# Performance work log

Measured on AMD Instinct MI355X. Metric: run time of the kernel, lower is better.

## Reference

```python
import jax, jax.numpy as jnp
import numpy as np

N_NODES = 100000
N_EDGES = 1600000
DIM = 128
N_SEEDS = 15000


def _gcn_stack(edges, x, Ws):
    """Multi-layer GCN with sym-normalized edge-list aggregation, residual, ReLU.
    edges: [2, E] int; x: [N, d] float; Ws: list of [d, d] weights."""
    n = x.shape[0]
    loop = jnp.arange(n, dtype=edges.dtype)
    src = jnp.concatenate([edges[0], loop])  # add self-loops
    dst = jnp.concatenate([edges[1], loop])
    deg = jax.ops.segment_sum(jnp.ones(src.shape, x.dtype), dst, num_segments=n)
    dinv = jax.lax.rsqrt(deg)  # deg >= 1 thanks to self-loops
    norm = dinv[src] * dinv[dst]  # [E+N]
    for W in Ws:
        h = x @ W                                   # [N, d] dense transform
        msg = norm[:, None] * h[src]                # gather + scale, [E+N, d]
        agg = jax.ops.segment_sum(msg, dst, num_segments=n)  # scatter-add
        x = jax.nn.relu(agg + h)                    # residual + activation
    return x


def setup_inputs() -> dict:
    key = jax.random.key(0)
    ks = jax.random.split(key, 8)
    scale = 1.0 / np.sqrt(DIM)
    return {
        "sr_ent_seeds": jax.random.randint(ks[0], (N_SEEDS,), 0, N_NODES),
        "tg_ent_seeds": jax.random.randint(ks[1], (N_SEEDS,), 0, N_NODES),
        "edges_sr": jax.random.randint(ks[2], (2, N_EDGES), 0, N_NODES),
        "edges_tg": jax.random.randint(ks[3], (2, N_EDGES), 0, N_NODES),
        "embedding_sr": jax.random.normal(ks[4], (N_NODES, DIM), jnp.float32),
        "embedding_tg": jax.random.normal(ks[5], (N_NODES, DIM), jnp.float32),
        "W0": jax.random.normal(ks[6], (DIM, DIM), jnp.float32) * scale,
        "W1": jax.random.normal(ks[7], (DIM, DIM), jnp.float32) * scale,
    }


def reference(sr_ent_seeds, tg_ent_seeds, edges_sr, edges_tg,
              embedding_sr, embedding_tg, W0, W1):
    Ws = [W0, W1]
    sr_ent_hid = _gcn_stack(edges_sr, embedding_sr, Ws)
    tg_ent_hid = _gcn_stack(edges_tg, embedding_tg, Ws)
    sr_seed_hid = sr_ent_hid[sr_ent_seeds]
    tg_seed_hid = tg_ent_hid[tg_ent_seeds]
    return (sr_seed_hid, tg_seed_hid, sr_ent_hid, tg_ent_hid)
```

## Files before the change

kernel.cpp:

```cpp
#include <hip/hip_runtime.h>

#define NN 100000
#define NE 1600000
#define NT (2 * NN)
#define ET (2 * NE)
#define DIM 128
#define NS 15000
#define SB2 ((NT + 255) / 256)
#define PAD 136
#define NRANGE 8
#define RSZ (NT / NRANGE)
#define CH 32
#define CI4 (ET / 4 / CH)
#define NE4 (NE / 4)

typedef __attribute__((ext_vector_type(8))) short frag_ab;
typedef __attribute__((ext_vector_type(4))) float frag_cd;
typedef __attribute__((ext_vector_type(4))) int i4;

__device__ __forceinline__ unsigned short f2bf(float f) {
    unsigned int u = __float_as_uint(f);
    u += 0x7fff + ((u >> 16) & 1);
    return (unsigned short)(u >> 16);
}
__device__ __forceinline__ float bflo(unsigned int u) { return __uint_as_float(u << 16); }
__device__ __forceinline__ float bfhi(unsigned int u) { return __uint_as_float(u & 0xffff0000u); }

__global__ __launch_bounds__(1024) void hist_k(const int* __restrict__ e_sr,
                                               const int* __restrict__ e_tg,
                                               int* __restrict__ P) {
    __shared__ int lc[RSZ];
    const int r = blockIdx.x & (NRANGE - 1);
    const int c = blockIdx.x >> 3;
    const int lo = r * RSZ;
    for (int i = threadIdx.x; i < RSZ; i += 1024) lc[i] = 0;
    __syncthreads();
    const int base = c * CI4;
    for (int v = threadIdx.x; v < CI4; v += 1024) {
        i4 d4;
        if (c < 16) {
            d4 = *((const i4*)e_sr + NE4 + base + v);
        } else {
            d4 = *((const i4*)e_tg + base + v);
            d4 += NN;
        }
#pragma unroll
        for (int j = 0; j < 4; ++j) {
            const int t = d4[j] - lo;
            if ((unsigned)t < RSZ) atomicAdd(&lc[t], 1);
        }
    }
    __syncthreads();
    for (int i = threadIdx.x; i < RSZ; i += 1024) P[c * NT + lo + i] = lc[i];
}

__global__ __launch_bounds__(256) void reduceA_k(const int* __restrict__ P,
                                                 int* __restrict__ cnt,
                                                 float* __restrict__ dinv,
                                                 int* __restrict__ bsum) {
    __shared__ int sh[256];
    const int t = threadIdx.x;
    const int i = blockIdx.x * 256 + t;
    int s = 0;
    if (i < NT) {
#pragma unroll
        for (int c = 0; c < CH; ++c) s += P[c * NT + i];
        cnt[i] = s;
        dinv[i] = rsqrtf((float)(s + 1));
    }
    sh[t] = s;
    __syncthreads();
    for (int off = 128; off > 0; off >>= 1) {
        if (t < off) sh[t] += sh[t + off];
        __syncthreads();
    }
    if (t == 0) bsum[blockIdx.x] = sh[0];
}

__global__ __launch_bounds__(1024) void scanB_k(int* bsum, int* row_ptr) {
    __shared__ int s[1024];
    const int t = threadIdx.x;
    const int v = (t < SB2) ? bsum[t] : 0;
    s[t] = v;
    __syncthreads();
    for (int off = 1; off < 1024; off <<= 1) {
        int add = (t >= off) ? s[t - off] : 0;
        __syncthreads();
        s[t] += add;
        __syncthreads();
    }
    if (t < SB2) bsum[t] = s[t] - v;
    if (t == SB2 - 1) row_ptr[NT] = s[t];
}

__global__ __launch_bounds__(256) void scanCbase_k(const int* __restrict__ cnt,
                                                   const int* __restrict__ bsum,
                                                   int* __restrict__ row_ptr,
                                                   int* __restrict__ P) {
    __shared__ int s[256];
    const int t = threadIdx.x;
    const int i = blockIdx.x * 256 + t;
    const int v = (i < NT) ? cnt[i] : 0;
    s[t] = v;
    __syncthreads();
    for (int off = 1; off < 256; off <<= 1) {
        int add = (t >= off) ? s[t - off] : 0;
        __syncthreads();
        s[t] += add;
        __syncthreads();
    }
    if (i < NT) {
        const int rp = bsum[blockIdx.x] + s[t] - v;
        row_ptr[i] = rp;
        int run = rp;
#pragma unroll
        for (int c = 0; c < CH; ++c) {
            const int pv = P[c * NT + i];
            P[c * NT + i] = run;
            run += pv;
        }
    }
}

__global__ __launch_bounds__(1024) void fillp_k(const int* __restrict__ e_sr,
                                                const int* __restrict__ e_tg,
                                                const int* __restrict__ P,
                                                int* __restrict__ csr_src) {
    __shared__ int cur[RSZ];
    const int r = blockIdx.x & (NRANGE - 1);
    const int c = blockIdx.x >> 3;
    const int lo = r * RSZ;
    for (int i = threadIdx.x; i < RSZ; i += 1024) cur[i] = P[c * NT + lo + i];
    __syncthreads();
    const int base = c * CI4;
    for (int v = threadIdx.x; v < CI4; v += 1024) {
        i4 s4, d4;
        if (c < 16) {
            s4 = *((const i4*)e_sr + base + v);
            d4 = *((const i4*)e_sr + NE4 + base + v);
        } else {
            s4 = *((const i4*)e_tg + base + v - NE4);
            d4 = *((const i4*)e_tg + base + v);
            s4 += NN;
            d4 += NN;
        }
#pragma unroll
        for (int j = 0; j < 4; ++j) {
            const int t = d4[j] - lo;
            if ((unsigned)t < RSZ) {
                const int pos = atomicAdd(&cur[t], 1);
                csr_src[pos] = s4[j];
            }
        }
    }
}

__global__ __launch_bounds__(256) void convW2_k(const float* __restrict__ W0,
                                                const float* __restrict__ W1,
                                                unsigned short* __restrict__ wt0,
                                                unsigned short* __restrict__ wt1) {
    int i = blockIdx.x * 256 + threadIdx.x;
    if (i >= 2 * DIM * DIM) return;
    const float* W = (i < DIM * DIM) ? W0 : W1;
    unsigned short* wt = (i < DIM * DIM) ? wt0 : wt1;
    const int ii = i & (DIM * DIM - 1);
    const int n = ii & 127, k = ii >> 7;
    wt[n * DIM + k] = f2bf(W[k * DIM + n]);
}

__global__ __launch_bounds__(256) void gemmE_k(const float* __restrict__ emb_sr,
                                               const float* __restrict__ emb_tg,
                                               const unsigned short* __restrict__ Wt,
                                               const float* __restrict__ dinv,
                                               unsigned short* __restrict__ Gb) {
    __shared__ unsigned short xs[64 * PAD];
    __shared__ unsigned short ws[128 * PAD];
    const int tid = threadIdx.x;
    const int row0 = blockIdx.x * 64;

    for (int i = tid; i < 128 * 16; i += 256) {
        const int r = i >> 4, o = i & 15;
        *(uint4*)&ws[r * PAD + o * 8] = *(const uint4*)&Wt[r * DIM + o * 8];
    }
    for (int i = tid; i < 64 * 32; i += 256) {
        const int r = i >> 5, o = i & 31;
        const int gr = row0 + r;
        const float4 v = (gr < NN) ? ((const float4*)emb_sr)[gr * 32 + o]
                                   : ((const float4*)emb_tg)[(gr - NN) * 32 + o];
        ushort4 b;
        b.x = f2bf(v.x); b.y = f2bf(v.y); b.z = f2bf(v.z); b.w = f2bf(v.w);
        *(ushort4*)&xs[r * PAD + o * 4] = b;
    }
    __syncthreads();

    const int wave = tid >> 6;
    const int lane = tid & 63;
    const int m = lane & 15;
    const int quad = lane >> 4;
    const int rbase = wave * 16;

    frag_cd acc[8];
#pragma unroll
    for (int ct = 0; ct < 8; ct++) acc[ct] = (frag_cd){0.f, 0.f, 0.f, 0.f};

#pragma unroll
    for (int ks = 0; ks < 4; ks++) {
        const frag_ab a = *(const frag_ab*)&xs[(rbase + m) * PAD + ks * 32 + quad * 8];
#pragma unroll
        for (int ct = 0; ct < 8; ct++) {
            const frag_ab b = *(const frag_ab*)&ws[(ct * 16 + m) * PAD + ks * 32 + quad * 8];
            acc[ct] = __builtin_amdgcn_mfma_f32_16x16x32_bf16(a, b, acc[ct], 0, 0, 0);
        }
    }

#pragma unroll
    for (int r = 0; r < 4; r++) {
        const int grow = row0 + rbase + quad * 4 + r;
        const float dv = dinv[grow];
#pragma unroll
        for (int ct = 0; ct < 8; ct++)
            Gb[grow * DIM + ct * 16 + m] = f2bf(dv * acc[ct][r]);
    }
}

__global__ __launch_bounds__(256) void gemm_mfma_k(const unsigned short* __restrict__ Xb,
                                                   const unsigned short* __restrict__ Wt,
                                                   const float* __restrict__ dinv,
                                                   unsigned short* __restrict__ Gb) {
    __shared__ unsigned short xs[64 * PAD];
    __shared__ unsigned short ws[128 * PAD];
    const int tid = threadIdx.x;
    const int row0 = blockIdx.x * 64;

    for (int i = tid; i < 128 * 16; i += 256) {
        const int r = i >> 4, o = i & 15;
        *(uint4*)&ws[r * PAD + o * 8] = *(const uint4*)&Wt[r * DIM + o * 8];
    }
    for (int i = tid; i < 64 * 16; i += 256) {
        const int r = i >> 4, o = i & 15;
        *(uint4*)&xs[r * PAD + o * 8] = *(const uint4*)&Xb[(row0 + r) * DIM + o * 8];
    }
    __syncthreads();

    const int wave = tid >> 6;
    const int lane = tid & 63;
    const int m = lane & 15;
    const int quad = lane >> 4;
    const int rbase = wave * 16;

    frag_cd acc[8];
#pragma unroll
    for (int ct = 0; ct < 8; ct++) acc[ct] = (frag_cd){0.f, 0.f, 0.f, 0.f};

#pragma unroll
    for (int ks = 0; ks < 4; ks++) {
        const frag_ab a = *(const frag_ab*)&xs[(rbase + m) * PAD + ks * 32 + quad * 8];
#pragma unroll
        for (int ct = 0; ct < 8; ct++) {
            const frag_ab b = *(const frag_ab*)&ws[(ct * 16 + m) * PAD + ks * 32 + quad * 8];
            acc[ct] = __builtin_amdgcn_mfma_f32_16x16x32_bf16(a, b, acc[ct], 0, 0, 0);
        }
    }

#pragma unroll
    for (int r = 0; r < 4; r++) {
        const int grow = row0 + rbase + quad * 4 + r;
        const float dv = dinv[grow];
#pragma unroll
        for (int ct = 0; ct < 8; ct++)
            Gb[grow * DIM + ct * 16 + m] = f2bf(dv * acc[ct][r]);
    }
}

template <bool OUT_BF16>
__global__ __launch_bounds__(256) void pull_k(const int* __restrict__ row_ptr,
                                              const int* __restrict__ csr_src,
                                              const float* __restrict__ dinv,
                                              const unsigned short* __restrict__ Gb,
                                              float* __restrict__ outf,
                                              unsigned short* __restrict__ outb) {
    const int node = (blockIdx.x * 256 + threadIdx.x) >> 6;
    if (node >= NT) return;
    const int lane = threadIdx.x & 63;
    const unsigned int* __restrict__ G2 = (const unsigned int*)Gb;

    const int beg = row_ptr[node];
    const int end = row_ptr[node + 1];
    const float d = dinv[node];
    const float sq = 1.0f / d;

    const unsigned int gu = G2[node * 64 + lane];
    float sx = bflo(gu);
    float sy = bfhi(gu);
    const float hx = sx * sq;
    const float hy = sy * sq;

    for (int base = beg; base < end; base += 64) {
        int rem = end - base; if (rem > 64) rem = 64;
        const int sl = (lane < rem) ? csr_src[base + lane] : 0;
        int j = 0;
        for (; j + 16 <= rem; j += 16) {
            int ss[16];
            unsigned int mm[16];
#pragma unroll
            for (int q = 0; q < 16; ++q) ss[q] = __shfl(sl, j + q);
#pragma unroll
            for (int q = 0; q < 16; ++q) mm[q] = G2[ss[q] * 64 + lane];
#pragma unroll
            for (int q = 0; q < 16; ++q) { sx += bflo(mm[q]); sy += bfhi(mm[q]); }
        }
        for (; j + 8 <= rem; j += 8) {
            int ss[8];
            unsigned int mm[8];
#pragma unroll
            for (int q = 0; q < 8; ++q) ss[q] = __shfl(sl, j + q);
#pragma unroll
            for (int q = 0; q < 8; ++q) mm[q] = G2[ss[q] * 64 + lane];
#pragma unroll
            for (int q = 0; q < 8; ++q) { sx += bflo(mm[q]); sy += bfhi(mm[q]); }
        }
        for (; j + 4 <= rem; j += 4) {
            int ss[4];
            unsigned int mm[4];
#pragma unroll
            for (int q = 0; q < 4; ++q) ss[q] = __shfl(sl, j + q);
#pragma unroll
            for (int q = 0; q < 4; ++q) mm[q] = G2[ss[q] * 64 + lane];
#pragma unroll
            for (int q = 0; q < 4; ++q) { sx += bflo(mm[q]); sy += bfhi(mm[q]); }
        }
        for (; j < rem; ++j) {
            const int s = __shfl(sl, j);
            const unsigned int mu = G2[s * 64 + lane];
            sx += bflo(mu);
            sy += bfhi(mu);
        }
    }
    const float ax = fmaxf(d * sx + hx, 0.f);
    const float ay = fmaxf(d * sy + hy, 0.f);
    if (OUT_BF16) {
        ((unsigned int*)outb)[node * 64 + lane] =
            (unsigned int)f2bf(ax) | ((unsigned int)f2bf(ay) << 16);
    } else {
        float2 o; o.x = ax; o.y = ay;
        ((float2*)outf)[node * 64 + lane] = o;
    }
}

__global__ __launch_bounds__(256) void gather2_k(const int* __restrict__ sr_seeds,
                                                 const int* __restrict__ tg_seeds,
                                                 const float* __restrict__ ent,
                                                 float* __restrict__ sr_out,
                                                 float* __restrict__ tg_out) {
    const int gid = blockIdx.x * 256 + threadIdx.x;
    const int s = gid >> 5;
    if (s >= 2 * NS) return;
    const int q = gid & 31;
    const bool tg = s >= NS;
    const int si = tg ? s - NS : s;
    const int node = tg ? tg_seeds[si] + NN : sr_seeds[si];
    float* o = tg ? tg_out : sr_out;
    ((float4*)o)[si * 32 + q] = ((const float4*)ent)[node * 32 + q];
}

extern "C" void kernel_launch(void* const* d_in, const int* in_sizes, int n_in,
                              void* d_out, int out_size, void* d_ws, size_t ws_size,
                              hipStream_t stream) {
    const int* sr_seeds = (const int*)d_in[0];
    const int* tg_seeds = (const int*)d_in[1];
    const int* edges_sr = (const int*)d_in[2];
    const int* edges_tg = (const int*)d_in[3];
    const float* emb_sr = (const float*)d_in[4];
    const float* emb_tg = (const float*)d_in[5];
    const float* W0 = (const float*)d_in[6];
    const float* W1 = (const float*)d_in[7];
    float* out = (float*)d_out;

    int* cnt = (int*)d_ws;
    float* dinv = (float*)(cnt + 200704);
    int* row_ptr = (int*)(dinv + 200704);
    int* bsum = row_ptr + 200704;
    int* csr_src = bsum + 1024;
    unsigned short* wt0 = (unsigned short*)(csr_src + ET);
    unsigned short* wt1 = wt0 + DIM * DIM;
    unsigned short* hb = wt1 + DIM * DIM;
    int* P = (int*)hb;

    float* sr_seed_out = out;
    float* tg_seed_out = out + (long long)NS * DIM;
    float* ent = out + (long long)2 * NS * DIM;
    unsigned short* xb = (unsigned short*)ent;

    const int gGemm = (NT + 63) / 64;
    const int gPull = NT / 4;

    convW2_k<<<(2 * DIM * DIM + 255) / 256, 256, 0, stream>>>(W0, W1, wt0, wt1);

    hist_k<<<NRANGE * CH, 1024, 0, stream>>>(edges_sr, edges_tg, P);
    reduceA_k<<<SB2, 256, 0, stream>>>(P, cnt, dinv, bsum);
    scanB_k<<<1, 1024, 0, stream>>>(bsum, row_ptr);
    scanCbase_k<<<SB2, 256, 0, stream>>>(cnt, bsum, row_ptr, P);
    fillp_k<<<NRANGE * CH, 1024, 0, stream>>>(edges_sr, edges_tg, P, csr_src);

    gemmE_k<<<gGemm, 256, 0, stream>>>(emb_sr, emb_tg, wt0, dinv, hb);
    pull_k<true><<<gPull, 256, 0, stream>>>(row_ptr, csr_src, dinv, hb, nullptr, xb);
    gemm_mfma_k<<<gGemm, 256, 0, stream>>>(xb, wt1, dinv, hb);
    pull_k<false><<<gPull, 256, 0, stream>>>(row_ptr, csr_src, dinv, hb, ent, nullptr);

    const int gSeed = (2 * NS * 32 + 255) / 256;
    gather2_k<<<gSeed, 256, 0, stream>>>(sr_seeds, tg_seeds, ent, sr_seed_out, tg_seed_out);
}
```

Baseline: 579.2 us.

## Pre-bucket edges by destination range before histogram and CSR fill

Adds a bucketing pass that partitions all edges into 16 destination-range buckets, packing the local destination and the source into one word. The histogram and fill kernels then read only their own bucket instead of each scanning every edge and discarding out-of-range ones. This cuts the redundant global reads that came from NRANGE-fold edge scans, at the cost of an extra kernel, a global atomic per block, and a fixed bucket capacity assumption (BCAP). The packing relies on sources fitting in 18 bits and local destinations fitting in the upper bits.

```diff
diff --git a/kernel.cpp b/kernel.cpp
--- a/kernel.cpp
+++ b/kernel.cpp
@@ -8,10 +8,10 @@
 #define NS 15000
 #define SB2 ((NT + 255) / 256)
 #define PAD 136
-#define NRANGE 8
+#define NRANGE 16
 #define RSZ (NT / NRANGE)
-#define CH 32
-#define CI4 (ET / 4 / CH)
+#define CH 16
+#define BCAP 210000
 #define NE4 (NE / 4)
 
 typedef __attribute__((ext_vector_type(8))) short frag_ab;
@@ -26,29 +26,67 @@
 __device__ __forceinline__ float bflo(unsigned int u) { return __uint_as_float(u << 16); }
 __device__ __forceinline__ float bfhi(unsigned int u) { return __uint_as_float(u & 0xffff0000u); }
 
-__global__ __launch_bounds__(1024) void hist_k(const int* __restrict__ e_sr,
-                                               const int* __restrict__ e_tg,
+__global__ __launch_bounds__(256) void bucket_k(const int* __restrict__ e_sr,
+                                                const int* __restrict__ e_tg,
+                                                int* __restrict__ gcur,
+                                                int* __restrict__ bkt) {
+    __shared__ int bcnt[4][NRANGE];
+    __shared__ int bbase[4][NRANGE];
+    const int tid = threadIdx.x;
+    if (tid < 4 * NRANGE) ((int*)bcnt)[tid] = 0;
+    __syncthreads();
+    const int g = blockIdx.x * 256 + tid;
+    i4 s4, d4;
+    if (g < NE4) {
+        s4 = *((const i4*)e_sr + g);
+        d4 = *((const i4*)e_sr + NE4 + g);
+    } else {
+        s4 = *((const i4*)e_tg + g - NE4);
+        d4 = *((const i4*)e_tg + g);
+        s4 += NN;
+        d4 += NN;
+    }
+    const int wv = tid >> 6;
+    int rr[4], lr[4];
+#pragma unroll
+    for (int j = 0; j < 4; ++j) {
+        rr[j] = d4[j] / RSZ;
+        lr[j] = atomicAdd(&bcnt[wv][rr[j]], 1);
+    }
+    __syncthreads();
+    if (tid < NRANGE) {
+        const int t0 = bcnt[0][tid], t1 = bcnt[1][tid];
+        const int t2 = bcnt[2][tid], t3 = bcnt[3][tid];
+        const int b = atomicAdd(&gcur[tid], t0 + t1 + t2 + t3);
+        bbase[0][tid] = b;
+        bbase[1][tid] = b + t0;
+        bbase[2][tid] = b + t0 + t1;
+        bbase[3][tid] = b + t0 + t1 + t2;
+    }
+    __syncthreads();
+#pragma unroll
+    for (int j = 0; j < 4; ++j) {
+        const int dtl = d4[j] - rr[j] * RSZ;
+        bkt[bbase[wv][rr[j]] + lr[j]] = (dtl << 18) | s4[j];
+    }
+}
+
+__global__ __launch_bounds__(1024) void hist_k(const int* __restrict__ gcur,
+                                               const int* __restrict__ bkt,
                                                int* __restrict__ P) {
     __shared__ int lc[RSZ];
     const int r = blockIdx.x & (NRANGE - 1);
-    const int c = blockIdx.x >> 3;
+    const int c = blockIdx.x >> 4;
     const int lo = r * RSZ;
     for (int i = threadIdx.x; i < RSZ; i += 1024) lc[i] = 0;
     __syncthreads();
-    const int base = c * CI4;
-    for (int v = threadIdx.x; v < CI4; v += 1024) {
-        i4 d4;
-        if (c < 16) {
-            d4 = *((const i4*)e_sr + NE4 + base + v);
-        } else {
-            d4 = *((const i4*)e_tg + base + v);
-            d4 += NN;
-        }
-#pragma unroll
-        for (int j = 0; j < 4; ++j) {
-            const int t = d4[j] - lo;
-            if ((unsigned)t < RSZ) atomicAdd(&lc[t], 1);
-        }
+    const int n_r = gcur[r] - r * BCAP;
+    const int S = (n_r + CH - 1) / CH;
+    const int s0 = c * S;
+    int s1 = s0 + S; if (s1 > n_r) s1 = n_r;
+    for (int v = s0 + threadIdx.x; v < s1; v += 1024) {
+        const unsigned int w = (unsigned int)bkt[r * BCAP + v];
+        atomicAdd(&lc[w >> 18], 1);
     }
     __syncthreads();
     for (int i = threadIdx.x; i < RSZ; i += 1024) P[c * NT + lo + i] = lc[i];
@@ -122,44 +160,34 @@
     }
 }
 
-__global__ __launch_bounds__(1024) void fillp_k(const int* __restrict__ e_sr,
-                                                const int* __restrict__ e_tg,
+__global__ __launch_bounds__(1024) void fillp_k(const int* __restrict__ gcur,
+                                                const int* __restrict__ bkt,
                                                 const int* __restrict__ P,
                                                 int* __restrict__ csr_src) {
     __shared__ int cur[RSZ];
     const int r = blockIdx.x & (NRANGE - 1);
-    const int c = blockIdx.x >> 3;
+    const int c = blockIdx.x >> 4;
     const int lo = r * RSZ;
     for (int i = threadIdx.x; i < RSZ; i += 1024) cur[i] = P[c * NT + lo + i];
     __syncthreads();
-    const int base = c * CI4;
-    for (int v = threadIdx.x; v < CI4; v += 1024) {
-        i4 s4, d4;
-        if (c < 16) {
-            s4 = *((const i4*)e_sr + base + v);
-            d4 = *((const i4*)e_sr + NE4 + base + v);
-        } else {
-            s4 = *((const i4*)e_tg + base + v - NE4);
-            d4 = *((const i4*)e_tg + base + v);
-            s4 += NN;
-            d4 += NN;
-        }
-#pragma unroll
-        for (int j = 0; j < 4; ++j) {
-            const int t = d4[j] - lo;
-            if ((unsigned)t < RSZ) {
-                const int pos = atomicAdd(&cur[t], 1);
-                csr_src[pos] = s4[j];
-            }
-        }
+    const int n_r = gcur[r] - r * BCAP;
+    const int S = (n_r + CH - 1) / CH;
+    const int s0 = c * S;
+    int s1 = s0 + S; if (s1 > n_r) s1 = n_r;
+    for (int v = s0 + threadIdx.x; v < s1; v += 1024) {
+        const unsigned int w = (unsigned int)bkt[r * BCAP + v];
+        const int pos = atomicAdd(&cur[w >> 18], 1);
+        csr_src[pos] = (int)(w & 0x3FFFFu);
     }
 }
 
 __global__ __launch_bounds__(256) void convW2_k(const float* __restrict__ W0,
                                                 const float* __restrict__ W1,
                                                 unsigned short* __restrict__ wt0,
-                                                unsigned short* __restrict__ wt1) {
+                                                unsigned short* __restrict__ wt1,
+                                                int* __restrict__ gcur) {
     int i = blockIdx.x * 256 + threadIdx.x;
+    if (blockIdx.x == 0 && threadIdx.x < NRANGE) gcur[threadIdx.x] = threadIdx.x * BCAP;
     if (i >= 2 * DIM * DIM) return;
     const float* W = (i < DIM * DIM) ? W0 : W1;
     unsigned short* wt = (i < DIM * DIM) ? wt0 : wt1;
@@ -385,6 +413,8 @@
     unsigned short* wt1 = wt0 + DIM * DIM;
     unsigned short* hb = wt1 + DIM * DIM;
     int* P = (int*)hb;
+    int* bkt = P + CH * NT;
+    int* gcur = bsum + 800;
 
     float* sr_seed_out = out;
     float* tg_seed_out = out + (long long)NS * DIM;
@@ -393,14 +423,17 @@
 
     const int gGemm = (NT + 63) / 64;
     const int gPull = NT / 4;
-
-    convW2_k<<<(2 * DIM * DIM + 255) / 256, 256, 0, stream>>>(W0, W1, wt0, wt1);
-
-    hist_k<<<NRANGE * CH, 1024, 0, stream>>>(edges_sr, edges_tg, P);
+    const int gBkt = ET / 1024;
+    const int gHF = NRANGE * CH;
+
+    convW2_k<<<(2 * DIM * DIM + 255) / 256, 256, 0, stream>>>(W0, W1, wt0, wt1, gcur);
+
+    bucket_k<<<gBkt, 256, 0, stream>>>(edges_sr, edges_tg, gcur, bkt);
+    hist_k<<<gHF, 1024, 0, stream>>>(gcur, bkt, P);
     reduceA_k<<<SB2, 256, 0, stream>>>(P, cnt, dinv, bsum);
     scanB_k<<<1, 1024, 0, stream>>>(bsum, row_ptr);
     scanCbase_k<<<SB2, 256, 0, stream>>>(cnt, bsum, row_ptr, P);
-    fillp_k<<<NRANGE * CH, 1024, 0, stream>>>(edges_sr, edges_tg, P, csr_src);
+    fillp_k<<<gHF, 1024, 0, stream>>>(gcur, bkt, P, csr_src);
 
     gemmE_k<<<gGemm, 256, 0, stream>>>(emb_sr, emb_tg, wt0, dinv, hb);
     pull_k<true><<<gPull, 256, 0, stream>>>(row_ptr, csr_src, dinv, hb, nullptr, xb);
```

Measured after the change: 564.5 us. 2.5% less time.
